# Kernel optimization log

Measured on AMD Instinct MI355X. Metric: run time of the kernel, lower is better.

Reference implementation:

```python
import jax, jax.numpy as jnp
import numpy as np

D_MODEL = 512
D_STATE = 128
D_CONV = 4
EXPAND = 2
HEADDIM = 64
D_INNER = EXPAND * D_MODEL            # 1024
NHEADS = D_INNER // HEADDIM           # 16
CONV_DIM = D_INNER + 2 * D_STATE      # 1280
D_IN_PROJ = 2 * D_INNER + 2 * D_STATE + NHEADS  # 2320
EPS = 1e-5


def _mamba2(u, in_w, conv_w, conv_b, A_log, dt_bias, Dp, norm_w, out_w):
    # u: [b, l, d_model]  -- Mamba2 forward (ngroups=1), SSD in exact quadratic form
    b, l, _ = u.shape
    zxbcdt = u @ in_w.T                                   # [b,l,2320]
    z = zxbcdt[..., :D_INNER]
    xBC = zxbcdt[..., D_INNER:D_INNER + CONV_DIM]
    dt = zxbcdt[..., D_INNER + CONV_DIM:]                 # [b,l,nheads]
    # causal depthwise conv1d (kernel 4) + silu
    xp = jnp.pad(xBC, ((0, 0), (D_CONV - 1, 0), (0, 0)))
    conv = sum(xp[:, k:k + l, :] * conv_w[:, k] for k in range(D_CONV))
    xBC = jax.nn.silu(conv + conv_b)
    x = xBC[..., :D_INNER].reshape(b, l, NHEADS, HEADDIM)
    Bm = xBC[..., D_INNER:D_INNER + D_STATE]              # [b,l,d_state]
    Cm = xBC[..., D_INNER + D_STATE:]                     # [b,l,d_state]
    dt = jax.nn.softplus(dt + dt_bias)                    # [b,l,nheads]
    dtA = dt * (-jnp.exp(A_log))                          # [b,l,nheads], negative
    # SSD quadratic (semiseparable) form: L[t,s] = exp(sum_{r=s+1..t} dtA_r), causal
    cs = jnp.cumsum(dtA, axis=1)                          # [b,l,nh]
    seg = cs[:, :, None, :] - cs[:, None, :, :]           # [b,t,s,nh]
    mask = jnp.tril(jnp.ones((l, l), bool))
    L = jnp.exp(jnp.where(mask[None, :, :, None], seg, -jnp.inf))
    G = jnp.einsum('btd,bsd->bts', Cm, Bm)                # C_t . B_s
    dtx = dt[..., None] * x                               # [b,l,nh,hd]
    y = jnp.einsum('btsn,bsnp->btnp', G[..., None] * L, dtx)
    y = (y + x * Dp[:, None]).reshape(b, l, D_INNER)      # D skip
    # gated RMSNorm (norm_before_gate=False): rmsnorm(y * silu(z)) * weight
    y = y * jax.nn.silu(z)
    y = y * jax.lax.rsqrt(jnp.mean(jnp.square(y), -1, keepdims=True) + EPS) * norm_w
    return y @ out_w.T


def _forward(x, h_in_w, h_conv_w, h_conv_b, h_A_log, h_dt_bias, h_D, h_norm_w, h_out_w,
             v_in_w, v_conv_w, v_conv_b, v_A_log, v_dt_bias, v_D, v_norm_w, v_out_w,
             fc_w, fc_b):
    B, H, W, C = x.shape
    hp = (h_in_w, h_conv_w, h_conv_b, h_A_log, h_dt_bias, h_D, h_norm_w, h_out_w)
    vp = (v_in_w, v_conv_w, v_conv_b, v_A_log, v_dt_bias, v_D, v_norm_w, v_out_w)
    # horizontal: scan along W for each (B*H) row
    xh = x.reshape(-1, W, C)
    h1 = _mamba2(xh, *hp)
    # NOTE: original code flips dim 0 (batch), reproduced faithfully
    h2 = jnp.flip(_mamba2(jnp.flip(xh, 0), *hp), 0)
    h = jnp.concatenate([h1, h2], -1).reshape(B, H, W, -1)
    # vertical: scan along H for each (B*W) column
    xv = jnp.transpose(x, (0, 2, 1, 3)).reshape(-1, H, C)
    v1 = _mamba2(xv, *vp)
    v2 = jnp.flip(_mamba2(jnp.flip(xv, 0), *vp), 0)
    v = jnp.transpose(jnp.concatenate([v1, v2], -1).reshape(B, W, H, -1), (0, 2, 1, 3))
    out = jnp.concatenate([v, h], -1) @ fc_w.T + fc_b     # [B,H,W,C]
    return out


def setup_inputs() -> dict:
    key = jax.random.key(0)
    ks = jax.random.split(key, 8)
    B, H, W, C = 2, 64, 64, D_MODEL
    x = jax.random.normal(ks[0], (B, H, W, C), jnp.float32)

    def mk(k):
        kk = jax.random.split(k, 5)
        return {
            'in_w': 0.02 * jax.random.normal(kk[0], (D_IN_PROJ, D_MODEL), jnp.float32),
            'conv_w': 0.1 * jax.random.normal(kk[1], (CONV_DIM, D_CONV), jnp.float32),
            'conv_b': jnp.zeros((CONV_DIM,), jnp.float32),
            'A_log': jnp.log(jax.random.uniform(kk[2], (NHEADS,), jnp.float32, 1.0, 16.0)),
            'dt_bias': jnp.log(jnp.expm1(jax.random.uniform(kk[3], (NHEADS,), jnp.float32, 1e-3, 0.1))),
            'D': jnp.ones((NHEADS,), jnp.float32),
            'norm_w': jnp.ones((D_INNER,), jnp.float32),
            'out_w': 0.02 * jax.random.normal(kk[4], (D_MODEL, D_INNER), jnp.float32),
        }

    hp, vp = mk(ks[1]), mk(ks[2])
    inp = {'x': x}
    inp.update({f'h_{n}': v for n, v in hp.items()})
    inp.update({f'v_{n}': v for n, v in vp.items()})
    inp['fc_w'] = 0.02 * jax.random.normal(ks[3], (D_MODEL, 4 * D_MODEL), jnp.float32)
    inp['fc_b'] = jnp.zeros((D_MODEL,), jnp.float32)
    return inp


def reference(x, h_in_w, h_conv_w, h_conv_b, h_A_log, h_dt_bias, h_D, h_norm_w, h_out_w,
              v_in_w, v_conv_w, v_conv_b, v_A_log, v_dt_bias, v_D, v_norm_w, v_out_w,
              fc_w, fc_b):
    return _forward(x, h_in_w, h_conv_w, h_conv_b, h_A_log, h_dt_bias, h_D, h_norm_w, h_out_w,
                    v_in_w, v_conv_w, v_conv_b, v_A_log, v_dt_bias, v_D, v_norm_w, v_out_w,
                    fc_w, fc_b)
```

## Files before the change

kernel.cpp:

```cpp
#include <hip/hip_runtime.h>

#define NROWS 8192
#define NZX   2304
#define BCS   136
#define XMS   72

#define PB0 4096
#define PB1 (PB0 + 2048)
#define PB2 (PB1 + 2304)
#define PB3 (PB2 + 256)
#define PB4 (PB3 + 1024)

typedef __attribute__((ext_vector_type(8))) short bf16x8;
typedef __attribute__((ext_vector_type(4))) float f32x4;

__device__ __forceinline__ float bf2f(unsigned short u) {
    union { unsigned int i; float f; } v; v.i = ((unsigned int)u) << 16; return v.f;
}
__device__ __forceinline__ unsigned short f2bf(float f) {
    union { float f; unsigned int i; } v; v.f = f;
    return (unsigned short)((v.i + 0x8000u) >> 16);
}

__device__ __forceinline__ void async_lds16(const unsigned short* g, unsigned short* l) {
    __builtin_amdgcn_global_load_lds(
        (const __attribute__((address_space(1))) unsigned int*)g,
        (__attribute__((address_space(3))) unsigned int*)l, 16, 0, 0);
}

__global__ __launch_bounds__(256) void prep_kernel(
    const float* __restrict__ x, const float* __restrict__ fcw,
    const float* __restrict__ iw0, const float* __restrict__ iw1,
    const float* __restrict__ ow0, const float* __restrict__ ow1,
    const float* __restrict__ db0, const float* __restrict__ db1,
    const float* __restrict__ al0, const float* __restrict__ al1,
    unsigned short* __restrict__ xbf, unsigned short* __restrict__ wf,
    unsigned short* __restrict__ wbA, unsigned short* __restrict__ wbOT0,
    unsigned short* __restrict__ wbOT1, float* __restrict__ dtbb,
    float* __restrict__ csbb)
{
    __shared__ char sm[27648] __attribute__((aligned(16)));
    const int blk = blockIdx.x, tid = threadIdx.x;
    if (blk < PB0) {
        int i = blk * 256 + tid;
        float4 v = *(const float4*)(x + (size_t)i * 4);
        ushort4 o;
        o.x = f2bf(v.x); o.y = f2bf(v.y); o.z = f2bf(v.z); o.w = f2bf(v.w);
        *(ushort4*)(xbf + (size_t)i * 4) = o;
    } else if (blk < PB1) {
        int idx = (blk - PB0) * 256 + tid;
        int o = idx >> 10, c = idx & 1023;
        int half = c >> 9, cc = c & 511;
        float v = fcw[(size_t)o * 2048 + half * 1024 + cc] +
                  fcw[(size_t)o * 2048 + half * 1024 + 512 + cc];
        wf[idx] = f2bf(v);
    } else if (blk < PB2) {
        int local = blk - PB1;
        int dir = local / 1152;
        int i = (local % 1152) * 256 + tid;
        const float* s = dir ? iw1 : iw0;
        float4 v = *(const float4*)(s + (size_t)i * 4);
        ushort4 o;
        o.x = f2bf(v.x); o.y = f2bf(v.y); o.z = f2bf(v.z); o.w = f2bf(v.w);
        *(ushort4*)(wbA + (size_t)dir * (2304 * 512) + (size_t)i * 4) = o;
    } else if (blk < PB3) {
        float (*T)[65] = (float(*)[65])sm;
        int local = blk - PB2;
        int z = local >> 7, rem = local & 127;
        const float* s = z ? ow1 : ow0;
        unsigned short* d = z ? wbOT1 : wbOT0;
        const int bo = (rem >> 4) * 64, bc = (rem & 15) * 64;
#pragma unroll
        for (int i = 0; i < 16; ++i) {
            int slot = tid + i * 256;
            int r = slot >> 6, c = slot & 63;
            T[r][c] = s[(size_t)(bo + r) * 1024 + bc + c];
        }
        __syncthreads();
#pragma unroll
        for (int i = 0; i < 16; ++i) {
            int slot = tid + i * 256;
            int cr = slot >> 6, oc = slot & 63;
            d[(size_t)(bc + cr) * 512 + bo + oc] = f2bf(T[oc][cr]);
        }
    } else {
        float (*wsm)[512] = (float(*)[512])sm;
        float (*xs)[68]   = (float(*)[68])(sm + 8192);
        float (*dta)[64]  = (float(*)[64])(sm + 8192 + 17408);
        float (*dtt)[64]  = (float(*)[64])(sm + 8192 + 17408 + 1024);
        int local = blk - PB3;
        const int dir = local >> 9, bxl = local & 511;
        const float* in_w = dir ? iw1 : iw0;
        const float* dt_bias = dir ? db1 : db0;
        const float* A_log = dir ? al1 : al0;
        float* dtb = dtbb + (size_t)dir * 131072;
        float* csb = csbb + (size_t)dir * 131072;
        const int seq = bxl >> 2, hq = bxl & 3;
#pragma unroll
        for (int i = 0; i < 2; ++i) {
            int slot = tid + i * 256;
            int h = slot >> 7, c = (slot & 127) * 4;
            *(float4*)&wsm[h][c] = *(const float4*)(in_w + (size_t)(2304 + hq * 4 + h) * 512 + c);
        }
        const int t = tid & 63, hh = tid >> 6;
        const int h = hq * 4 + hh;
        float acc = 0.f;
        for (int c0 = 0; c0 < 512; c0 += 64) {
            __syncthreads();
#pragma unroll
            for (int i = 0; i < 4; ++i) {
                int slot = tid + i * 256;
                int r = slot >> 4, cc = (slot & 15) * 4;
                size_t row = (dir == 0) ? (size_t)seq * 64 + r
                                        : (size_t)(seq >> 6) * 4096 + (size_t)r * 64 + (seq & 63);
                *(float4*)&xs[r][cc] = *(const float4*)(x + row * 512 + c0 + cc);
            }
            __syncthreads();
#pragma unroll
            for (int cc = 0; cc < 64; cc += 4) {
                float4 u4 = *(const float4*)&xs[t][cc];
                const float* w = &wsm[hh][c0 + cc];
                acc += u4.x * w[0] + u4.y * w[1] + u4.z * w[2] + u4.w * w[3];
            }
        }
        float v = acc + dt_bias[h];
        float dtv = (v > 20.f) ? v : log1pf(__expf(v));
        dtt[hh][t] = dtv;
        dta[hh][t] = dtv * -__expf(A_log[h]);
        __syncthreads();
        if (tid < 4) {
            float run = 0.f;
            int ob = (seq * 16 + hq * 4 + tid) * 64;
            for (int tt = 0; tt < 64; ++tt) {
                run += dta[tid][tt];
                dtb[ob + tt] = dtt[tid][tt];
                csb[ob + tt] = run;
            }
        }
    }
}

__global__ __launch_bounds__(256) void gemm_phase(
    const unsigned short* __restrict__ xbf, const unsigned short* __restrict__ wbA,
    unsigned short* __restrict__ zx, const unsigned short* __restrict__ wf,
    const unsigned short* __restrict__ wbOT0, const unsigned short* __restrict__ wbOT1,
    unsigned short* __restrict__ wcomb)
{
    __shared__ unsigned short SMEM[8192];
    unsigned short* As = SMEM;
    unsigned short* Bs = SMEM + 4096;
    const int bx = blockIdx.x, by = blockIdx.y, z = blockIdx.z;
    const unsigned short *A, *B;
    unsigned short* C;
    int lda, ldb, ldc, perm, mB, nB;
    if (bx < 64) {
        A = xbf; lda = 512; perm = z;
        B = wbA + (size_t)z * (2304 * 512); ldb = 512;
        C = zx + (size_t)z * NROWS * NZX; ldc = NZX;
        mB = bx * 128; nB = by * 128;
    } else {
        if (by >= 8) return;
        A = z ? wf : wf + 512; lda = 1024; perm = 0;
        B = z ? wbOT1 : wbOT0; ldb = 512;
        C = z ? wcomb : wcomb + 1024; ldc = 2048;
        mB = (bx - 64) * 128; nB = by * 128;
    }
    const int tid = threadIdx.x, wave = tid >> 6, lane = tid & 63;
    const int wm = (wave >> 1) * 64, wn = (wave & 1) * 64;
    const int lr = lane & 15, lq = lane >> 4;
    const int s0 = wave * 64 + lane, s1 = s0 + 256;
    const int row0 = s0 >> 2, q0 = (s0 & 3) ^ ((row0 >> 1) & 3);
    const int row1 = s1 >> 2, q1 = (s1 & 3) ^ ((row1 >> 1) & 3);
    int ar0 = mB + row0, ar1 = mB + row1;
    if (perm) {
        ar0 = (ar0 & ~4095) | ((ar0 & 63) << 6) | ((ar0 >> 6) & 63);
        ar1 = (ar1 & ~4095) | ((ar1 & 63) << 6) | ((ar1 >> 6) & 63);
    }
    const unsigned short* Ag0 = A + (size_t)ar0 * lda + q0 * 8;
    const unsigned short* Ag1 = A + (size_t)ar1 * lda + q1 * 8;
    const unsigned short* Bg0 = B + (size_t)(nB + row0) * ldb + q0 * 8;
    const unsigned short* Bg1 = B + (size_t)(nB + row1) * ldb + q1 * 8;
    unsigned short* lA0 = As + s0 * 8; unsigned short* lA1 = As + s1 * 8;
    unsigned short* lB0 = Bs + s0 * 8; unsigned short* lB1 = Bs + s1 * 8;
    const int sw = (lq ^ ((lr >> 1) & 3)) * 8;
    int aoff[4], boff[4];
#pragma unroll
    for (int i = 0; i < 4; ++i) {
        aoff[i] = (wm + i * 16 + lr) * 32 + sw;
        boff[i] = (wn + i * 16 + lr) * 32 + sw;
    }
    f32x4 zero4 = {0.f,0.f,0.f,0.f};
    f32x4 acc[4][4] = {{zero4,zero4,zero4,zero4},{zero4,zero4,zero4,zero4},
                       {zero4,zero4,zero4,zero4},{zero4,zero4,zero4,zero4}};
    for (int k0 = 0; k0 < 512; k0 += 32) {
        async_lds16(Ag0 + k0, lA0);
        async_lds16(Ag1 + k0, lA1);
        async_lds16(Bg0 + k0, lB0);
        async_lds16(Bg1 + k0, lB1);
        __syncthreads();
        bf16x8 a[4], b[4];
#pragma unroll
        for (int i = 0; i < 4; ++i) a[i] = *(const bf16x8*)(As + aoff[i]);
#pragma unroll
        for (int i = 0; i < 4; ++i) b[i] = *(const bf16x8*)(Bs + boff[i]);
#pragma unroll
        for (int mi = 0; mi < 4; ++mi)
#pragma unroll
            for (int ni = 0; ni < 4; ++ni)
                acc[mi][ni] = __builtin_amdgcn_mfma_f32_16x16x32_bf16(
                    a[mi], b[ni], acc[mi][ni], 0, 0, 0);
        __syncthreads();
    }
    unsigned short* WR = SMEM + wave * 1024;
#pragma unroll
    for (int mi = 0; mi < 4; ++mi) {
#pragma unroll
        for (int ni = 0; ni < 4; ++ni) {
#pragma unroll
            for (int r = 0; r < 4; ++r) {
                int r16 = lq * 4 + r;
                int cn = ni * 16 + lr;
                int gp = ((cn >> 3) + (r16 >> 1)) & 7;
                WR[r16 * 64 + gp * 8 + (cn & 7)] = f2bf(acc[mi][ni][r]);
            }
        }
#pragma unroll
        for (int j = 0; j < 2; ++j) {
            int r16 = j * 8 + (lane >> 3);
            int gr = lane & 7;
            int gp = (gr + (r16 >> 1)) & 7;
            uint4 v = *(const uint4*)(WR + r16 * 64 + gp * 8);
            int row = mB + wm + mi * 16 + r16;
            *(uint4*)(C + (size_t)row * ldc + nB + wn + gr * 8) = v;
        }
    }
}

__global__ __launch_bounds__(256) void gemm_final2048(
    const unsigned short* __restrict__ YV, const unsigned short* __restrict__ YH,
    const unsigned short* __restrict__ W, const float* __restrict__ bias,
    float* __restrict__ C)
{
    __shared__ unsigned short As[128 * 32];
    __shared__ unsigned short Bs[64 * 32];
    const int tid = threadIdx.x, wave = tid >> 6, lane = tid & 63;
    const int mB = blockIdx.x * 128, nB = blockIdx.y * 64;
    const int lr = lane & 15, lq = lane >> 4;
    const int sA0 = tid, sA1 = tid + 256;
    const int rA0 = sA0 >> 2, qA0 = ((sA0 & 3) ^ ((rA0 >> 1) & 3)) * 8;
    const int rA1 = sA1 >> 2, qA1 = ((sA1 & 3) ^ ((rA1 >> 1) & 3)) * 8;
    const int rB  = tid >> 2, qB  = ((tid & 3) ^ ((rB >> 1) & 3)) * 8;
    const int g0r = mB + rA0, g1r = mB + rA1;
    const int p0r = (g0r & ~4095) | ((g0r & 63) << 6) | ((g0r >> 6) & 63);
    const int p1r = (g1r & ~4095) | ((g1r & 63) << 6) | ((g1r >> 6) & 63);
    const unsigned short* Bg = W + (size_t)(nB + rB) * 2048 + qB;
    unsigned short* lA0 = As + sA0 * 8; unsigned short* lA1 = As + sA1 * 8;
    unsigned short* lB  = Bs + tid * 8;
    const int sw = (lq ^ ((lr >> 1) & 3)) * 8;
    int aoff[2], boff[4];
#pragma unroll
    for (int i = 0; i < 2; ++i) aoff[i] = (wave * 32 + i * 16 + lr) * 32 + sw;
#pragma unroll
    for (int i = 0; i < 4; ++i) boff[i] = (i * 16 + lr) * 32 + sw;
    f32x4 zero4 = {0.f,0.f,0.f,0.f};
    f32x4 acc[2][4] = {{zero4,zero4,zero4,zero4},{zero4,zero4,zero4,zero4}};
    for (int k0 = 0; k0 < 2048; k0 += 32) {
        int kk0 = k0 + qA0, kk1 = k0 + qA1;
        const unsigned short* g0 = (kk0 < 1024) ? YV + (size_t)p0r * 1024 + kk0
                                                : YH + (size_t)g0r * 1024 + (kk0 - 1024);
        const unsigned short* g1 = (kk1 < 1024) ? YV + (size_t)p1r * 1024 + kk1
                                                : YH + (size_t)g1r * 1024 + (kk1 - 1024);
        async_lds16(g0, lA0);
        async_lds16(g1, lA1);
        async_lds16(Bg + k0, lB);
        __syncthreads();
        bf16x8 a[2], b[4];
#pragma unroll
        for (int i = 0; i < 2; ++i) a[i] = *(const bf16x8*)(As + aoff[i]);
#pragma unroll
        for (int i = 0; i < 4; ++i) b[i] = *(const bf16x8*)(Bs + boff[i]);
#pragma unroll
        for (int mi = 0; mi < 2; ++mi)
#pragma unroll
            for (int ni = 0; ni < 4; ++ni)
                acc[mi][ni] = __builtin_amdgcn_mfma_f32_16x16x32_bf16(
                    a[mi], b[ni], acc[mi][ni], 0, 0, 0);
        __syncthreads();
    }
    const int rbase = lq * 4;
#pragma unroll
    for (int mi = 0; mi < 2; ++mi)
#pragma unroll
        for (int ni = 0; ni < 4; ++ni) {
            int col = nB + ni * 16 + lr;
            float bb = bias[col];
#pragma unroll
            for (int r = 0; r < 4; ++r) {
                int row = mB + wave * 32 + mi * 16 + rbase + r;
                C[(size_t)row * 512 + col] = acc[mi][ni][r] + bb;
            }
        }
}

__global__ __launch_bounds__(320) void conv_silu(
    const unsigned short* __restrict__ zxb, const float* __restrict__ cw0,
    const float* __restrict__ cw1, const float* __restrict__ cb0,
    const float* __restrict__ cb1, unsigned short* __restrict__ xbcb)
{
    __shared__ unsigned short S[64 * 320];
    const int dir = blockIdx.y;
    const unsigned short* zx = zxb + (size_t)dir * NROWS * NZX;
    unsigned short* xbc = xbcb + (size_t)dir * NROWS * 1280;
    const float* cw = dir ? cw1 : cw0;
    const float* cb = dir ? cb1 : cb0;
    const int tid = threadIdx.x;
    const int seq = blockIdx.x >> 2, tile = blockIdx.x & 3;
    const int cbase = tile * 320;
    const unsigned short* src = zx + (size_t)seq * 64 * NZX + 1024 + cbase;
#pragma unroll
    for (int i = 0; i < 8; ++i) {
        int slot = tid + i * 320;
        int r = slot / 40, ch = (slot % 40) * 8;
        *(uint4*)(S + r * 320 + ch) = *(const uint4*)(src + (size_t)r * NZX + ch);
    }
    __syncthreads();
    const int c8 = (tid % 40) * 8, rg = tid / 40;
    const int gc = cbase + c8;
    float4 b0 = *(const float4*)(cb + gc), b1 = *(const float4*)(cb + gc + 4);
    const float bias[8] = {b0.x,b0.y,b0.z,b0.w,b1.x,b1.y,b1.z,b1.w};
    float4 wv[8];
#pragma unroll
    for (int j = 0; j < 8; ++j) wv[j] = *(const float4*)(cw + (size_t)(gc + j) * 4);
    unsigned short* dst = xbc + (size_t)seq * 64 * 1280 + gc;
#pragma unroll
    for (int r = 0; r < 8; ++r) {
        int t = rg * 8 + r;
        float acc[8];
#pragma unroll
        for (int j = 0; j < 8; ++j) acc[j] = bias[j];
#pragma unroll
        for (int k = 0; k < 4; ++k) {
            int ts = t + k - 3;
            if (ts >= 0) {
                uint4 xv = *(const uint4*)(S + ts * 320 + c8);
                const unsigned short* xs = (const unsigned short*)&xv;
#pragma unroll
                for (int j = 0; j < 8; ++j)
                    acc[j] += bf2f(xs[j]) * ((const float*)&wv[j])[k];
            }
        }
        unsigned short out8[8] __attribute__((aligned(16)));
#pragma unroll
        for (int j = 0; j < 8; ++j) out8[j] = f2bf(acc[j] / (1.f + __expf(-acc[j])));
        *(uint4*)(dst + (size_t)t * 1280) = *(const uint4*)out8;
    }
}

__global__ __launch_bounds__(256) void scan_kernel(
    const unsigned short* __restrict__ xbcb, const float* __restrict__ dtbb,
    const float* __restrict__ csbb, const float* __restrict__ Dv0,
    const float* __restrict__ Dv1, unsigned short* __restrict__ yh,
    unsigned short* __restrict__ yv)
{
    __shared__ unsigned short Bs[64 * BCS];
    __shared__ unsigned short Cs[64 * BCS];
    __shared__ unsigned short XsT[64 * XMS];
    __shared__ unsigned short Ms[64 * XMS];
    __shared__ float dts[64], css[64];
    const int dir = blockIdx.y;
    const unsigned short* xbc = xbcb + (size_t)dir * NROWS * 1280;
    const float* dtb = dtbb + (size_t)dir * 131072;
    const float* csb = csbb + (size_t)dir * 131072;
    const float* Dv = dir ? Dv1 : Dv0;
    unsigned short* y = dir ? yv : yh;
    const int tid = threadIdx.x;
    const int lane = tid & 63, wave = tid >> 6;
    const int seq = blockIdx.x >> 4, h = blockIdx.x & 15;
    if (tid < 64) {
        dts[tid] = dtb[(seq * 16 + h) * 64 + tid];
        css[tid] = csb[(seq * 16 + h) * 64 + tid];
    }
    const unsigned short* base = xbc + (size_t)seq * 64 * 1280;
#pragma unroll
    for (int i = 0; i < 4; ++i) {
        int e = (tid + i * 256) * 8;
        int r = e >> 7, c = e & 127;
        *(uint4*)(Bs + r * BCS + c) = *(const uint4*)(base + (size_t)r * 1280 + 1024 + c);
        *(uint4*)(Cs + r * BCS + c) = *(const uint4*)(base + (size_t)r * 1280 + 1152 + c);
    }
#pragma unroll
    for (int i = 0; i < 2; ++i) {
        int e = (tid + i * 256) * 8;
        int t = e >> 6, p0 = e & 63;
        uint4 xval = *(const uint4*)(base + (size_t)t * 1280 + h * 64 + p0);
        const unsigned short* xs = (const unsigned short*)&xval;
#pragma unroll
        for (int j = 0; j < 8; ++j) {
            int jl = (j + lane) & 7;
            XsT[(p0 + jl) * XMS + t] = xs[jl];
        }
    }
    __syncthreads();
    const int lr = lane & 15, lq = lane >> 4;
    f32x4 zero4 = {0.f,0.f,0.f,0.f};
    f32x4 acc[4] = {zero4, zero4, zero4, zero4};
#pragma unroll
    for (int kt = 0; kt < 4; ++kt) {
        bf16x8 a = *(const bf16x8*)(Cs + (wave * 16 + lr) * BCS + kt * 32 + lq * 8);
#pragma unroll
        for (int ni = 0; ni < 4; ++ni) {
            bf16x8 b = *(const bf16x8*)(Bs + (ni * 16 + lr) * BCS + kt * 32 + lq * 8);
            acc[ni] = __builtin_amdgcn_mfma_f32_16x16x32_bf16(a, b, acc[ni], 0, 0, 0);
        }
    }
    float css_t[4];
#pragma unroll
    for (int r = 0; r < 4; ++r) css_t[r] = css[wave * 16 + lq * 4 + r];
#pragma unroll
    for (int ni = 0; ni < 4; ++ni) {
        int s = ni * 16 + lr;
        float cs_s = css[s], dt_s = dts[s];
#pragma unroll
        for (int r = 0; r < 4; ++r) {
            int t = wave * 16 + lq * 4 + r;
            float e = __expf(fminf(css_t[r] - cs_s, 0.f));
            float m = (s <= t) ? acc[ni][r] * e * dt_s : 0.f;
            Ms[t * XMS + s] = f2bf(m);
        }
    }
    __syncthreads();
    f32x4 yacc[4] = {zero4, zero4, zero4, zero4};
#pragma unroll
    for (int kt = 0; kt < 2; ++kt) {
        bf16x8 a = *(const bf16x8*)(Ms + (wave * 16 + lr) * XMS + kt * 32 + lq * 8);
#pragma unroll
        for (int ni = 0; ni < 4; ++ni) {
            bf16x8 b = *(const bf16x8*)(XsT + (ni * 16 + lr) * XMS + kt * 32 + lq * 8);
            yacc[ni] = __builtin_amdgcn_mfma_f32_16x16x32_bf16(a, b, yacc[ni], 0, 0, 0);
        }
    }
    const float Dh = Dv[h];
    unsigned short* yout = y + (size_t)seq * 64 * 1024 + h * 64;
#pragma unroll
    for (int ni = 0; ni < 4; ++ni) {
        int p = ni * 16 + lr;
#pragma unroll
        for (int r = 0; r < 4; ++r) {
            int t = wave * 16 + lq * 4 + r;
            float v = yacc[ni][r] + Dh * bf2f(XsT[p * XMS + t]);
            yout[(size_t)t * 1024 + p] = f2bf(v);
        }
    }
}

__global__ __launch_bounds__(128) void gate_norm(
    const unsigned short* __restrict__ zxb, unsigned short* __restrict__ yh,
    unsigned short* __restrict__ yv, const float* __restrict__ nw0,
    const float* __restrict__ nw1)
{
    const int dir = blockIdx.y;
    const unsigned short* zx = zxb + (size_t)dir * NROWS * NZX;
    unsigned short* y = dir ? yv : yh;
    const float* nw = dir ? nw1 : nw0;
    const int row = blockIdx.x, tid = threadIdx.x;
    uint4 yv4 = *(const uint4*)(y + (size_t)row * 1024 + tid * 8);
    uint4 zv4 = *(const uint4*)(zx + (size_t)row * NZX + tid * 8);
    const unsigned short* ys = (const unsigned short*)&yv4;
    const unsigned short* zs = (const unsigned short*)&zv4;
    float g[8]; float ss = 0.f;
#pragma unroll
    for (int j = 0; j < 8; ++j) {
        float zv = bf2f(zs[j]);
        float gv = bf2f(ys[j]) * (zv / (1.f + __expf(-zv)));
        g[j] = gv; ss += gv * gv;
    }
#pragma unroll
    for (int off = 32; off > 0; off >>= 1) ss += __shfl_xor(ss, off, 64);
    __shared__ float red[2];
    if ((tid & 63) == 0) red[tid >> 6] = ss;
    __syncthreads();
    ss = red[0] + red[1];
    const float scale = rsqrtf(ss * (1.f / 1024.f) + 1e-5f);
    unsigned short out8[8] __attribute__((aligned(16)));
#pragma unroll
    for (int j = 0; j < 8; ++j) out8[j] = f2bf(g[j] * scale * nw[tid * 8 + j]);
    *(uint4*)(y + (size_t)row * 1024 + tid * 8) = *(const uint4*)out8;
}

extern "C" void kernel_launch(void* const* d_in, const int* in_sizes, int n_in,
                              void* d_out, int out_size, void* d_ws, size_t ws_size,
                              hipStream_t stream)
{
    (void)in_sizes; (void)n_in; (void)out_size; (void)ws_size;
    const float* x   = (const float*)d_in[0];
    const float* fcw = (const float*)d_in[17];
    const float* fcb = (const float*)d_in[18];
    const float* iw0 = (const float*)d_in[1];  const float* iw1 = (const float*)d_in[9];
    const float* cw0 = (const float*)d_in[2];  const float* cw1 = (const float*)d_in[10];
    const float* cb0 = (const float*)d_in[3];  const float* cb1 = (const float*)d_in[11];
    const float* al0 = (const float*)d_in[4];  const float* al1 = (const float*)d_in[12];
    const float* db0 = (const float*)d_in[5];  const float* db1 = (const float*)d_in[13];
    const float* Dv0 = (const float*)d_in[6];  const float* Dv1 = (const float*)d_in[14];
    const float* nw0 = (const float*)d_in[7];  const float* nw1 = (const float*)d_in[15];
    const float* ow0 = (const float*)d_in[8];  const float* ow1 = (const float*)d_in[16];

    char* ws = (char*)d_ws;
    size_t off = 0;
    auto alloc = [&](size_t bytes) {
        void* p = ws + off; off += (bytes + 255) & ~(size_t)255; return p;
    };
    unsigned short* xbf   = (unsigned short*)alloc((size_t)NROWS * 512 * 2);
    unsigned short* wbA   = (unsigned short*)alloc((size_t)2 * 2304 * 512 * 2);
    unsigned short* wbOT0 = (unsigned short*)alloc((size_t)1024 * 512 * 2);
    unsigned short* wbOT1 = (unsigned short*)alloc((size_t)1024 * 512 * 2);
    unsigned short* wf    = (unsigned short*)alloc((size_t)512 * 1024 * 2);
    unsigned short* wcomb = (unsigned short*)alloc((size_t)512 * 2048 * 2);
    unsigned short* zx    = (unsigned short*)alloc((size_t)2 * NROWS * NZX * 2);
    unsigned short* xbc   = (unsigned short*)alloc((size_t)2 * NROWS * 1280 * 2);
    float* dtb            = (float*)alloc((size_t)2 * 2048 * 64 * 4);
    float* csb            = (float*)alloc((size_t)2 * 2048 * 64 * 4);
    unsigned short* ybh   = (unsigned short*)alloc((size_t)NROWS * 1024 * 2);
    unsigned short* ybv   = (unsigned short*)alloc((size_t)NROWS * 1024 * 2);

    prep_kernel<<<PB4, 256, 0, stream>>>(x, fcw, iw0, iw1, ow0, ow1, db0, db1,
                                         al0, al1, xbf, wf, wbA, wbOT0, wbOT1,
                                         dtb, csb);
    gemm_phase<<<dim3(68, 18, 2), 256, 0, stream>>>(xbf, wbA, zx, wf,
                                                    wbOT0, wbOT1, wcomb);
    conv_silu<<<dim3(512, 2), 320, 0, stream>>>(zx, cw0, cw1, cb0, cb1, xbc);
    scan_kernel<<<dim3(2048, 2), 256, 0, stream>>>(xbc, dtb, csb, Dv0, Dv1, ybh, ybv);
    gate_norm<<<dim3(NROWS, 2), 128, 0, stream>>>(zx, ybh, ybv, nw0, nw1);
    gemm_final2048<<<dim3(64, 8), 256, 0, stream>>>(ybv, ybh, wcomb, fcb, (float*)d_out);
}
```

Measured before the change: 309.2 us.

## Deepen GEMM K-tiles to 64, widen dt-proj blocks, and stage SSD output stores

Both bf16 GEMM kernels (the in/out-proj phase and the final fc GEMM) now stage 64-wide K slices per iteration instead of 32. They use an 8-way XOR swizzle and run two MFMA sub-steps per barrier pair, which halves the number of synchronisations and async load rounds in exchange for doubled LDS use. The dt projection part of the prep kernel now handles 8 heads per block instead of 4, so it runs half as many blocks and reuses each staged x tile for twice as many heads. The SSD kernel writes its output tile to LDS first and then issues coalesced 16-byte global stores instead of scattered 2-byte stores. The extra LDS per block may lower occupancy.

Result: faster. 294.1 us (-4.9%).

```diff
diff --git a/kernel.cpp b/kernel.cpp
--- a/kernel.cpp
+++ b/kernel.cpp
@@ -9,7 +9,7 @@
 #define PB1 (PB0 + 2048)
 #define PB2 (PB1 + 2304)
 #define PB3 (PB2 + 256)
-#define PB4 (PB3 + 1024)
+#define PB4 (PB3 + 512)
 
 typedef __attribute__((ext_vector_type(8))) short bf16x8;
 typedef __attribute__((ext_vector_type(4))) float f32x4;
@@ -39,7 +39,7 @@
     unsigned short* __restrict__ wbOT1, float* __restrict__ dtbb,
     float* __restrict__ csbb)
 {
-    __shared__ char sm[27648] __attribute__((aligned(16)));
+    __shared__ char sm[37888] __attribute__((aligned(16)));
     const int blk = blockIdx.x, tid = threadIdx.x;
     if (blk < PB0) {
         int i = blk * 256 + tid;
@@ -85,26 +85,25 @@
         }
     } else {
         float (*wsm)[512] = (float(*)[512])sm;
-        float (*xs)[68]   = (float(*)[68])(sm + 8192);
-        float (*dta)[64]  = (float(*)[64])(sm + 8192 + 17408);
-        float (*dtt)[64]  = (float(*)[64])(sm + 8192 + 17408 + 1024);
+        float (*xs)[68]   = (float(*)[68])(sm + 16384);
+        float (*dta)[64]  = (float(*)[64])(sm + 16384 + 17408);
+        float (*dtt)[64]  = (float(*)[64])(sm + 16384 + 17408 + 2048);
         int local = blk - PB3;
-        const int dir = local >> 9, bxl = local & 511;
+        const int dir = local >> 8, bxl = local & 255;
         const float* in_w = dir ? iw1 : iw0;
         const float* dt_bias = dir ? db1 : db0;
         const float* A_log = dir ? al1 : al0;
         float* dtb = dtbb + (size_t)dir * 131072;
         float* csb = csbb + (size_t)dir * 131072;
-        const int seq = bxl >> 2, hq = bxl & 3;
-#pragma unroll
-        for (int i = 0; i < 2; ++i) {
+        const int seq = bxl >> 1, hq = bxl & 1;
+#pragma unroll
+        for (int i = 0; i < 4; ++i) {
             int slot = tid + i * 256;
             int h = slot >> 7, c = (slot & 127) * 4;
-            *(float4*)&wsm[h][c] = *(const float4*)(in_w + (size_t)(2304 + hq * 4 + h) * 512 + c);
-        }
-        const int t = tid & 63, hh = tid >> 6;
-        const int h = hq * 4 + hh;
-        float acc = 0.f;
+            *(float4*)&wsm[h][c] = *(const float4*)(in_w + (size_t)(2304 + hq * 8 + h) * 512 + c);
+        }
+        const int t = tid & 63, hg = tid >> 6;
+        float acc[2] = {0.f, 0.f};
         for (int c0 = 0; c0 < 512; c0 += 64) {
             __syncthreads();
 #pragma unroll
@@ -119,18 +118,25 @@
 #pragma unroll
             for (int cc = 0; cc < 64; cc += 4) {
                 float4 u4 = *(const float4*)&xs[t][cc];
-                const float* w = &wsm[hh][c0 + cc];
-                acc += u4.x * w[0] + u4.y * w[1] + u4.z * w[2] + u4.w * w[3];
+                const float* w0 = &wsm[hg * 2][c0 + cc];
+                const float* w1 = &wsm[hg * 2 + 1][c0 + cc];
+                acc[0] += u4.x * w0[0] + u4.y * w0[1] + u4.z * w0[2] + u4.w * w0[3];
+                acc[1] += u4.x * w1[0] + u4.y * w1[1] + u4.z * w1[2] + u4.w * w1[3];
             }
         }
-        float v = acc + dt_bias[h];
-        float dtv = (v > 20.f) ? v : log1pf(__expf(v));
-        dtt[hh][t] = dtv;
-        dta[hh][t] = dtv * -__expf(A_log[h]);
+#pragma unroll
+        for (int hh = 0; hh < 2; ++hh) {
+            int hl = hg * 2 + hh;
+            int h = hq * 8 + hl;
+            float v = acc[hh] + dt_bias[h];
+            float dtv = (v > 20.f) ? v : log1pf(__expf(v));
+            dtt[hl][t] = dtv;
+            dta[hl][t] = dtv * -__expf(A_log[h]);
+        }
         __syncthreads();
-        if (tid < 4) {
+        if (tid < 8) {
             float run = 0.f;
-            int ob = (seq * 16 + hq * 4 + tid) * 64;
+            int ob = (seq * 16 + hq * 8 + tid) * 64;
             for (int tt = 0; tt < 64; ++tt) {
                 run += dta[tid][tt];
                 dtb[ob + tt] = dtt[tid][tt];
@@ -146,9 +152,9 @@
     const unsigned short* __restrict__ wbOT0, const unsigned short* __restrict__ wbOT1,
     unsigned short* __restrict__ wcomb)
 {
-    __shared__ unsigned short SMEM[8192];
+    __shared__ unsigned short SMEM[16384];
     unsigned short* As = SMEM;
-    unsigned short* Bs = SMEM + 4096;
+    unsigned short* Bs = SMEM + 8192;
     const int bx = blockIdx.x, by = blockIdx.y, z = blockIdx.z;
     const unsigned short *A, *B;
     unsigned short* C;
@@ -168,47 +174,53 @@
     const int tid = threadIdx.x, wave = tid >> 6, lane = tid & 63;
     const int wm = (wave >> 1) * 64, wn = (wave & 1) * 64;
     const int lr = lane & 15, lq = lane >> 4;
-    const int s0 = wave * 64 + lane, s1 = s0 + 256;
-    const int row0 = s0 >> 2, q0 = (s0 & 3) ^ ((row0 >> 1) & 3);
-    const int row1 = s1 >> 2, q1 = (s1 & 3) ^ ((row1 >> 1) & 3);
-    int ar0 = mB + row0, ar1 = mB + row1;
-    if (perm) {
-        ar0 = (ar0 & ~4095) | ((ar0 & 63) << 6) | ((ar0 >> 6) & 63);
-        ar1 = (ar1 & ~4095) | ((ar1 & 63) << 6) | ((ar1 >> 6) & 63);
-    }
-    const unsigned short* Ag0 = A + (size_t)ar0 * lda + q0 * 8;
-    const unsigned short* Ag1 = A + (size_t)ar1 * lda + q1 * 8;
-    const unsigned short* Bg0 = B + (size_t)(nB + row0) * ldb + q0 * 8;
-    const unsigned short* Bg1 = B + (size_t)(nB + row1) * ldb + q1 * 8;
-    unsigned short* lA0 = As + s0 * 8; unsigned short* lA1 = As + s1 * 8;
-    unsigned short* lB0 = Bs + s0 * 8; unsigned short* lB1 = Bs + s1 * 8;
-    const int sw = (lq ^ ((lr >> 1) & 3)) * 8;
-    int aoff[4], boff[4];
+    const unsigned short* AgP[4];
+    const unsigned short* BgP[4];
+    unsigned short* lA[4];
+    unsigned short* lB[4];
 #pragma unroll
     for (int i = 0; i < 4; ++i) {
-        aoff[i] = (wm + i * 16 + lr) * 32 + sw;
-        boff[i] = (wn + i * 16 + lr) * 32 + sw;
+        int s = tid + i * 256;
+        int r = s >> 3, p = s & 7;
+        int q = p ^ (r & 7);
+        int ar = mB + r;
+        if (perm) ar = (ar & ~4095) | ((ar & 63) << 6) | ((ar >> 6) & 63);
+        AgP[i] = A + (size_t)ar * lda + q * 8;
+        BgP[i] = B + (size_t)(nB + r) * ldb + q * 8;
+        lA[i] = As + s * 8;
+        lB[i] = Bs + s * 8;
+    }
+    const int aswz = lr & 7;
+    int arb[4], brb[4];
+#pragma unroll
+    for (int i = 0; i < 4; ++i) {
+        arb[i] = (wm + i * 16 + lr) * 64;
+        brb[i] = (wn + i * 16 + lr) * 64;
     }
     f32x4 zero4 = {0.f,0.f,0.f,0.f};
     f32x4 acc[4][4] = {{zero4,zero4,zero4,zero4},{zero4,zero4,zero4,zero4},
                        {zero4,zero4,zero4,zero4},{zero4,zero4,zero4,zero4}};
-    for (int k0 = 0; k0 < 512; k0 += 32) {
-        async_lds16(Ag0 + k0, lA0);
-        async_lds16(Ag1 + k0, lA1);
-        async_lds16(Bg0 + k0, lB0);
-        async_lds16(Bg1 + k0, lB1);
+    for (int k0 = 0; k0 < 512; k0 += 64) {
+#pragma unroll
+        for (int i = 0; i < 4; ++i) async_lds16(AgP[i] + k0, lA[i]);
+#pragma unroll
+        for (int i = 0; i < 4; ++i) async_lds16(BgP[i] + k0, lB[i]);
         __syncthreads();
-        bf16x8 a[4], b[4];
-#pragma unroll
-        for (int i = 0; i < 4; ++i) a[i] = *(const bf16x8*)(As + aoff[i]);
-#pragma unroll
-        for (int i = 0; i < 4; ++i) b[i] = *(const bf16x8*)(Bs + boff[i]);
-#pragma unroll
-        for (int mi = 0; mi < 4; ++mi)
-#pragma unroll
-            for (int ni = 0; ni < 4; ++ni)
-                acc[mi][ni] = __builtin_amdgcn_mfma_f32_16x16x32_bf16(
-                    a[mi], b[ni], acc[mi][ni], 0, 0, 0);
+#pragma unroll
+        for (int kh = 0; kh < 2; ++kh) {
+            const int ksw = ((kh * 4 + lq) ^ aswz) * 8;
+            bf16x8 a[4], b[4];
+#pragma unroll
+            for (int i = 0; i < 4; ++i) a[i] = *(const bf16x8*)(As + arb[i] + ksw);
+#pragma unroll
+            for (int i = 0; i < 4; ++i) b[i] = *(const bf16x8*)(Bs + brb[i] + ksw);
+#pragma unroll
+            for (int mi = 0; mi < 4; ++mi)
+#pragma unroll
+                for (int ni = 0; ni < 4; ++ni)
+                    acc[mi][ni] = __builtin_amdgcn_mfma_f32_16x16x32_bf16(
+                        a[mi], b[ni], acc[mi][ni], 0, 0, 0);
+        }
         __syncthreads();
     }
     unsigned short* WR = SMEM + wave * 1024;
@@ -241,50 +253,68 @@
     const unsigned short* __restrict__ W, const float* __restrict__ bias,
     float* __restrict__ C)
 {
-    __shared__ unsigned short As[128 * 32];
-    __shared__ unsigned short Bs[64 * 32];
+    __shared__ unsigned short As[128 * 64];
+    __shared__ unsigned short Bs[64 * 64];
     const int tid = threadIdx.x, wave = tid >> 6, lane = tid & 63;
     const int mB = blockIdx.x * 128, nB = blockIdx.y * 64;
     const int lr = lane & 15, lq = lane >> 4;
-    const int sA0 = tid, sA1 = tid + 256;
-    const int rA0 = sA0 >> 2, qA0 = ((sA0 & 3) ^ ((rA0 >> 1) & 3)) * 8;
-    const int rA1 = sA1 >> 2, qA1 = ((sA1 & 3) ^ ((rA1 >> 1) & 3)) * 8;
-    const int rB  = tid >> 2, qB  = ((tid & 3) ^ ((rB >> 1) & 3)) * 8;
-    const int g0r = mB + rA0, g1r = mB + rA1;
-    const int p0r = (g0r & ~4095) | ((g0r & 63) << 6) | ((g0r >> 6) & 63);
-    const int p1r = (g1r & ~4095) | ((g1r & 63) << 6) | ((g1r >> 6) & 63);
-    const unsigned short* Bg = W + (size_t)(nB + rB) * 2048 + qB;
-    unsigned short* lA0 = As + sA0 * 8; unsigned short* lA1 = As + sA1 * 8;
-    unsigned short* lB  = Bs + tid * 8;
-    const int sw = (lq ^ ((lr >> 1) & 3)) * 8;
-    int aoff[2], boff[4];
-#pragma unroll
-    for (int i = 0; i < 2; ++i) aoff[i] = (wave * 32 + i * 16 + lr) * 32 + sw;
-#pragma unroll
-    for (int i = 0; i < 4; ++i) boff[i] = (i * 16 + lr) * 32 + sw;
+    int aq[4], agr[4], apr[4];
+    unsigned short* lA[4];
+    const unsigned short* BgP[2];
+    unsigned short* lB[2];
+#pragma unroll
+    for (int i = 0; i < 4; ++i) {
+        int s = tid + i * 256;
+        int r = s >> 3, p = s & 7;
+        aq[i] = (p ^ (r & 7)) * 8;
+        int gr = mB + r;
+        agr[i] = gr;
+        apr[i] = (gr & ~4095) | ((gr & 63) << 6) | ((gr >> 6) & 63);
+        lA[i] = As + s * 8;
+    }
+#pragma unroll
+    for (int i = 0; i < 2; ++i) {
+        int s = tid + i * 256;
+        int r = s >> 3, p = s & 7;
+        int q = p ^ (r & 7);
+        BgP[i] = W + (size_t)(nB + r) * 2048 + q * 8;
+        lB[i] = Bs + s * 8;
+    }
+    const int aswz = lr & 7;
+    int arb[2], brb[4];
+#pragma unroll
+    for (int i = 0; i < 2; ++i) arb[i] = (wave * 32 + i * 16 + lr) * 64;
+#pragma unroll
+    for (int i = 0; i < 4; ++i) brb[i] = (i * 16 + lr) * 64;
     f32x4 zero4 = {0.f,0.f,0.f,0.f};
     f32x4 acc[2][4] = {{zero4,zero4,zero4,zero4},{zero4,zero4,zero4,zero4}};
-    for (int k0 = 0; k0 < 2048; k0 += 32) {
-        int kk0 = k0 + qA0, kk1 = k0 + qA1;
-        const unsigned short* g0 = (kk0 < 1024) ? YV + (size_t)p0r * 1024 + kk0
-                                                : YH + (size_t)g0r * 1024 + (kk0 - 1024);
-        const unsigned short* g1 = (kk1 < 1024) ? YV + (size_t)p1r * 1024 + kk1
-                                                : YH + (size_t)g1r * 1024 + (kk1 - 1024);
-        async_lds16(g0, lA0);
-        async_lds16(g1, lA1);
-        async_lds16(Bg + k0, lB);
+    for (int k0 = 0; k0 < 2048; k0 += 64) {
+#pragma unroll
+        for (int i = 0; i < 4; ++i) {
+            int kk = k0 + aq[i];
+            const unsigned short* g = (kk < 1024)
+                ? YV + (size_t)apr[i] * 1024 + kk
+                : YH + (size_t)agr[i] * 1024 + (kk - 1024);
+            async_lds16(g, lA[i]);
+        }
+#pragma unroll
+        for (int i = 0; i < 2; ++i) async_lds16(BgP[i] + k0, lB[i]);
         __syncthreads();
-        bf16x8 a[2], b[4];
-#pragma unroll
-        for (int i = 0; i < 2; ++i) a[i] = *(const bf16x8*)(As + aoff[i]);
-#pragma unroll
-        for (int i = 0; i < 4; ++i) b[i] = *(const bf16x8*)(Bs + boff[i]);
-#pragma unroll
-        for (int mi = 0; mi < 2; ++mi)
-#pragma unroll
-            for (int ni = 0; ni < 4; ++ni)
-                acc[mi][ni] = __builtin_amdgcn_mfma_f32_16x16x32_bf16(
-                    a[mi], b[ni], acc[mi][ni], 0, 0, 0);
+#pragma unroll
+        for (int kh = 0; kh < 2; ++kh) {
+            const int ksw = ((kh * 4 + lq) ^ aswz) * 8;
+            bf16x8 a[2], b[4];
+#pragma unroll
+            for (int i = 0; i < 2; ++i) a[i] = *(const bf16x8*)(As + arb[i] + ksw);
+#pragma unroll
+            for (int i = 0; i < 4; ++i) b[i] = *(const bf16x8*)(Bs + brb[i] + ksw);
+#pragma unroll
+            for (int mi = 0; mi < 2; ++mi)
+#pragma unroll
+                for (int ni = 0; ni < 4; ++ni)
+                    acc[mi][ni] = __builtin_amdgcn_mfma_f32_16x16x32_bf16(
+                        a[mi], b[ni], acc[mi][ni], 0, 0, 0);
+        }
         __syncthreads();
     }
     const int rbase = lq * 4;
@@ -440,7 +470,6 @@
         }
     }
     const float Dh = Dv[h];
-    unsigned short* yout = y + (size_t)seq * 64 * 1024 + h * 64;
 #pragma unroll
     for (int ni = 0; ni < 4; ++ni) {
         int p = ni * 16 + lr;
@@ -448,8 +477,17 @@
         for (int r = 0; r < 4; ++r) {
             int t = wave * 16 + lq * 4 + r;
             float v = yacc[ni][r] + Dh * bf2f(XsT[p * XMS + t]);
-            yout[(size_t)t * 1024 + p] = f2bf(v);
-        }
+            Ms[t * XMS + p] = f2bf(v);
+        }
+    }
+    __syncthreads();
+    unsigned short* yout = y + (size_t)seq * 64 * 1024 + h * 64;
+#pragma unroll
+    for (int i = 0; i < 2; ++i) {
+        int slot = tid + i * 256;
+        int t = slot >> 3, pc = (slot & 7) * 8;
+        uint4 v = *(const uint4*)(Ms + t * XMS + pc);
+        *(uint4*)(yout + (size_t)t * 1024 + pc) = v;
     }
 }
 
```
